# Optimization experiments

Hardware: AMD Instinct MI355X
Metric: run time of the kernel (lower is better)

Reference implementation:

```python
import jax, jax.numpy as jnp
import numpy as np
from jax import lax

B, E, D, N, R, K = 4, 768, 1536, 16, 48, 4
H, W = 16, 16
L = H * W
NDIR = 4


def _perms():
    idx = np.arange(L)
    idx_v = np.arange(L).reshape(H, W).T.reshape(-1)  # column-major (vertical) scan order
    perms = [idx, idx[::-1].copy(), idx_v, idx_v[::-1].copy()]
    invs = [np.argsort(p) for p in perms]
    return [jnp.asarray(p) for p in perms], [jnp.asarray(p) for p in invs]

PERMS, INVS = _perms()


def setup_inputs() -> dict:
    key = jax.random.key(0)
    ks = jax.random.split(key, 10)
    hidden_states = jax.random.normal(ks[0], (B, L, E), jnp.float32)
    in_proj_w = jax.random.normal(ks[1], (2 * D, E), jnp.float32) * 0.02
    out_proj_w = jax.random.normal(ks[2], (E, D), jnp.float32) * 0.02
    conv_w = jax.random.normal(ks[3], (NDIR, D, K), jnp.float32) * 0.1
    conv_b = jax.random.normal(ks[4], (NDIR, D), jnp.float32) * 0.1
    xproj_w = jax.random.normal(ks[5], (NDIR, R + 2 * N, D), jnp.float32) * 0.02
    dt_init_std = R ** -0.5
    dtproj_w = jax.random.uniform(ks[6], (NDIR, D, R), jnp.float32, -dt_init_std, dt_init_std)
    dt = jnp.exp(jax.random.uniform(ks[7], (NDIR, D), jnp.float32)
                 * (np.log(0.1) - np.log(0.001)) + np.log(0.001))
    dt = jnp.clip(dt, 1e-4, None)
    dtproj_b = dt + jnp.log(-jnp.expm1(-dt))  # inverse-softplus init as in the module
    A_log = jnp.broadcast_to(
        jnp.log(jnp.arange(1, N + 1, dtype=jnp.float32))[None, None, :], (NDIR, D, N)).copy()
    D_param = jnp.ones((NDIR, D), jnp.float32)
    return dict(hidden_states=hidden_states, in_proj_w=in_proj_w, out_proj_w=out_proj_w,
                conv_w=conv_w, conv_b=conv_b, xproj_w=xproj_w, dtproj_w=dtproj_w,
                dtproj_b=dtproj_b, A_log=A_log, D_param=D_param)


def _mamba_dir(xz, cw, cb, xw, dtw, dtb, a_log, dpar):
    # xz: (B, 2D, L) in this direction's scan order
    x, z = xz[:, :D], xz[:, D:]
    # causal depthwise conv1d + SiLU (mamba_inner_fn conv path)
    x = lax.conv_general_dilated(x, cw[:, None, :], (1,), [(K - 1, 0)],
                                 feature_group_count=D,
                                 dimension_numbers=('NCH', 'OIH', 'NCH'))
    x = jax.nn.silu(x + cb[None, :, None])
    # x_proj -> dt, B, C
    x_dbl = jnp.einsum('bdl,kd->bkl', x, xw)
    dt, Bm, Cm = x_dbl[:, :R], x_dbl[:, R:R + N], x_dbl[:, R + N:]
    delta = jax.nn.softplus(jnp.einsum('brl,dr->bdl', dt, dtw) + dtb[None, :, None])
    A = -jnp.exp(a_log)                                  # (D, N)
    dA = jnp.exp(jnp.einsum('bdl,dn->lbdn', delta, A))   # (L, B, D, N)
    dBu = jnp.einsum('bdl,bnl,bdl->lbdn', delta, Bm, x)  # delta * B * u

    def step(h, inp):
        da, dbu = inp
        h = da * h + dbu
        return h, h

    h0 = jnp.zeros((x.shape[0], D, N), x.dtype)
    _, hs = lax.scan(step, h0, (dA, dBu))                # (L, B, D, N)
    y = jnp.einsum('lbdn,bnl->bdl', hs, Cm) + dpar[None, :, None] * x
    return y * jax.nn.silu(z)                            # gate, (B, D, L)


def reference(hidden_states, in_proj_w, out_proj_w, conv_w, conv_b,
              xproj_w, dtproj_w, dtproj_b, A_log, D_param):
    xz = jnp.einsum('ble,fe->bfl', hidden_states, in_proj_w)  # (B, 2D, L)
    out = jnp.zeros((hidden_states.shape[0], D, L), hidden_states.dtype)
    for i in range(NDIR):  # fixed small set of structurally distinct scan directions
        xz_i = xz[:, :, PERMS[i]]
        y = _mamba_dir(xz_i, conv_w[i], conv_b[i], xproj_w[i], dtproj_w[i],
                       dtproj_b[i], A_log[i], D_param[i])
        out = out + y[:, :, INVS[i]]  # multi_reverse then sum-fusion
    return jnp.einsum('bdl,ed->ble', out, out_proj_w)
```

## Files before the change

### kernel.cpp

```cpp
#include <hip/hip_runtime.h>
#include <hip/hip_bf16.h>

#define BI   4
#define LI   256
#define EI   768
#define DI   1536
#define NI   16
#define RI   48
#define KI   4
#define NDIRS 4
#define F2D  3072
#define MROWS 1024
#define LOG2E 1.4426950408889634f

typedef float    floatx2 __attribute__((ext_vector_type(2)));
typedef float    floatx4 __attribute__((ext_vector_type(4)));
typedef _Float16 halfx2  __attribute__((ext_vector_type(2)));
typedef _Float16 halfx4  __attribute__((ext_vector_type(4)));
typedef _Float16 halfx8  __attribute__((ext_vector_type(8)));

typedef __attribute__((address_space(3))) unsigned lds_u32;
typedef __attribute__((address_space(1))) const unsigned glb_u32;

__device__ __forceinline__ void load16(const _Float16* g, _Float16* l) {
    __builtin_amdgcn_global_load_lds((glb_u32*)g, (lds_u32*)l, 16, 0, 0);
}

__device__ __forceinline__ int perm_idx(int dir, int j) {
    switch (dir) {
        case 0:  return j;
        case 1:  return 255 - j;
        case 2:  return ((j & 15) << 4) | (j >> 4);
        default: return 255 - (((j & 15) << 4) | (j >> 4));
    }
}

template<int CTRL>
__device__ __forceinline__ float dpp_add(float p) {
    int t = __builtin_amdgcn_update_dpp(0, __builtin_bit_cast(int, p),
                                        CTRL, 0xf, 0xf, true);
    return p + __builtin_bit_cast(float, t);
}
__device__ __forceinline__ float grp8_sum(float p) {
    p = dpp_add<0xB1>(p);
    p = dpp_add<0x4E>(p);
    p = dpp_add<0x141>(p);
    return p;
}

template<int BM, int BN, int WGN, int FM, int FN>
__device__ __forceinline__ void gemm_core(const _Float16* __restrict__ Ah,
                                          const _Float16* __restrict__ Al, int lda,
                                          const _Float16* __restrict__ Bh,
                                          const _Float16* __restrict__ Bl, int ldb,
                                          int nChunks, _Float16* smem,
                                          floatx4 (&acc)[FM][FN]) {
    const int tid = threadIdx.x, lane = tid & 63, wave = tid >> 6;
    const int wave_m = wave / WGN, wave_n = wave % WGN;
    _Float16* sAh = smem;
    _Float16* sAl = smem + BM * 32;
    _Float16* sBh = smem + BM * 64;
    _Float16* sBl = smem + BM * 64 + BN * 32;
    const int rr = lane & 15, koff = (lane >> 4) * 8;
    const int arow = wave_m * FM * 16, brow = wave_n * FN * 16;

    for (int c = 0; c < nChunks; ++c) {
        for (int idx = tid; idx < BM * 4; idx += 256) {
            int r = idx >> 2, s = (idx & 3) * 8;
            load16(Ah + (size_t)r * lda + c * 32 + s, sAh + idx * 8);
            load16(Al + (size_t)r * lda + c * 32 + s, sAl + idx * 8);
        }
        for (int idx = tid; idx < BN * 4; idx += 256) {
            int r = idx >> 2, s = (idx & 3) * 8;
            load16(Bh + (size_t)r * ldb + c * 32 + s, sBh + idx * 8);
            load16(Bl + (size_t)r * ldb + c * 32 + s, sBl + idx * 8);
        }
        asm volatile("s_waitcnt vmcnt(0)" ::: "memory");
        __syncthreads();

        halfx8 ahf[FM], alf[FM], bhf[FN], blf[FN];
        #pragma unroll
        for (int i = 0; i < FM; ++i) {
            ahf[i] = *(const halfx8*)(sAh + (arow + i * 16 + rr) * 32 + koff);
            alf[i] = *(const halfx8*)(sAl + (arow + i * 16 + rr) * 32 + koff);
        }
        #pragma unroll
        for (int j = 0; j < FN; ++j) {
            bhf[j] = *(const halfx8*)(sBh + (brow + j * 16 + rr) * 32 + koff);
            blf[j] = *(const halfx8*)(sBl + (brow + j * 16 + rr) * 32 + koff);
        }
        #pragma unroll
        for (int i = 0; i < FM; ++i)
            #pragma unroll
            for (int j = 0; j < FN; ++j) {
                acc[i][j] = __builtin_amdgcn_mfma_f32_16x16x32_f16(ahf[i], bhf[j], acc[i][j], 0, 0, 0);
                acc[i][j] = __builtin_amdgcn_mfma_f32_16x16x32_f16(ahf[i], blf[j], acc[i][j], 0, 0, 0);
                acc[i][j] = __builtin_amdgcn_mfma_f32_16x16x32_f16(alf[i], bhf[j], acc[i][j], 0, 0, 0);
            }
        __syncthreads();
    }
}

__global__ __launch_bounds__(256) void k_splitall(
        const float* __restrict__ hs,  const float* __restrict__ wip,
        const float* __restrict__ wop, const float* __restrict__ xw,
        const float* __restrict__ dtw,
        _Float16* __restrict__ hsh,  _Float16* __restrict__ hsl,
        _Float16* __restrict__ wiph, _Float16* __restrict__ wipl,
        _Float16* __restrict__ woph, _Float16* __restrict__ wopl,
        _Float16* __restrict__ xwh,  _Float16* __restrict__ xwl,
        _Float16* __restrict__ dtwh, _Float16* __restrict__ dtwl) {
    int i4 = (blockIdx.x * 256 + threadIdx.x) * 4;
    floatx4 v;
    _Float16 *dh, *dl; int off;
    if (i4 < 786432)        { off = i4;           v = *(const floatx4*)(hs + off);  dh = hsh;  dl = hsl;  }
    else if (i4 < 3145728)  { off = i4 - 786432;  v = *(const floatx4*)(wip + off); dh = wiph; dl = wipl; }
    else if (i4 < 4325376)  { off = i4 - 3145728; v = *(const floatx4*)(wop + off); dh = woph; dl = wopl; }
    else if (i4 < 4816896)  { off = i4 - 4325376; v = *(const floatx4*)(xw + off);  dh = xwh;  dl = xwl;  }
    else {
        int t0 = i4 - 4816896;
        int col = t0 & 63, dr = t0 >> 6;
        floatx4 z = {0.f, 0.f, 0.f, 0.f};
        v = (col < 48) ? *(const floatx4*)(dtw + (size_t)dr * 48 + col) : z;
        dh = dtwh; dl = dtwl; off = t0;
    }
    halfx4 hh, hl;
    #pragma unroll
    for (int e = 0; e < 4; ++e) {
        _Float16 h = (_Float16)v[e];
        hh[e] = h; hl[e] = (_Float16)(v[e] - (float)h);
    }
    *(halfx4*)(dh + off) = hh;
    *(halfx4*)(dl + off) = hl;
}

__global__ __launch_bounds__(256) void k_inproj_t(const _Float16* __restrict__ Ah,
                                                  const _Float16* __restrict__ Al,
                                                  const _Float16* __restrict__ Bh,
                                                  const _Float16* __restrict__ Bl,
                                                  float* __restrict__ C) {
    __shared__ _Float16 smem[128 * 64 + 128 * 64];
    int row0 = blockIdx.x * 128, col0 = blockIdx.y * 128, k0 = blockIdx.z * 384;
    float* Cp = C + (size_t)blockIdx.z * MROWS * F2D;
    floatx4 acc[4][4] = {};
    gemm_core<128, 128, 2, 4, 4>(Ah + (size_t)row0 * EI + k0, Al + (size_t)row0 * EI + k0, EI,
                                 Bh + (size_t)col0 * EI + k0, Bl + (size_t)col0 * EI + k0, EI,
                                 12, smem, acc);
    int lane = threadIdx.x & 63, wave = threadIdx.x >> 6;
    int cc = lane & 15, q = lane >> 4;
    int rbase = row0 + (wave >> 1) * 64, cbase = col0 + (wave & 1) * 64;
    #pragma unroll
    for (int i = 0; i < 4; ++i)
        #pragma unroll
        for (int j = 0; j < 4; ++j)
            #pragma unroll
            for (int r = 0; r < 4; ++r)
                Cp[(size_t)(rbase + i * 16 + q * 4 + r) * F2D + cbase + j * 16 + cc] = acc[i][j][r];
}

__global__ __launch_bounds__(256) void k_outproj_t(const _Float16* __restrict__ Ah,
                                                   const _Float16* __restrict__ Al,
                                                   const _Float16* __restrict__ Bh,
                                                   const _Float16* __restrict__ Bl,
                                                   float* __restrict__ C) {
    __shared__ _Float16 smem[192 * 64];
    int row0 = blockIdx.x * 64, col0 = blockIdx.y * 128, k0 = blockIdx.z * 384;
    float* Cp = C + (size_t)blockIdx.z * MROWS * EI;
    floatx4 acc[2][4] = {};
    gemm_core<64, 128, 2, 2, 4>(Ah + (size_t)row0 * DI + k0, Al + (size_t)row0 * DI + k0, DI,
                                Bh + (size_t)col0 * DI + k0, Bl + (size_t)col0 * DI + k0, DI,
                                12, smem, acc);
    int lane = threadIdx.x & 63, wave = threadIdx.x >> 6;
    int cc = lane & 15, q = lane >> 4;
    int rbase = row0 + (wave >> 1) * 32, cbase = col0 + (wave & 1) * 64;
    #pragma unroll
    for (int i = 0; i < 2; ++i)
        #pragma unroll
        for (int j = 0; j < 4; ++j)
            #pragma unroll
            for (int r = 0; r < 4; ++r)
                Cp[(size_t)(rbase + i * 16 + q * 4 + r) * EI + cbase + j * 16 + cc] = acc[i][j][r];
}

__global__ __launch_bounds__(256) void k_osum(const float* __restrict__ oacc,
                                              float* __restrict__ out) {
    int i4 = (blockIdx.x * 256 + threadIdx.x) * 4;
    const size_t S = (size_t)MROWS * EI;
    floatx4 s = *(const floatx4*)(oacc + i4) + *(const floatx4*)(oacc + S + i4) +
                *(const floatx4*)(oacc + 2 * S + i4) + *(const floatx4*)(oacc + 3 * S + i4);
    *(floatx4*)(out + i4) = s;
}

__global__ __launch_bounds__(256) void k_xdbl_t(const _Float16* __restrict__ xh,
                                                const _Float16* __restrict__ xl,
                                                const _Float16* __restrict__ xwh,
                                                const _Float16* __restrict__ xwl,
                                                float* __restrict__ C) {
    __shared__ _Float16 smem[208 * 64];
    int row0 = blockIdx.x * 128, dir = blockIdx.y, k0 = blockIdx.z * 192;
    float* Cp = C + (size_t)blockIdx.z * NDIRS * MROWS * 80;
    floatx4 acc[2][5] = {};
    const size_t abase = ((size_t)dir * MROWS + row0) * DI + k0;
    const size_t bbase = (size_t)dir * 80 * DI + k0;
    gemm_core<128, 80, 1, 2, 5>(xh + abase, xl + abase, DI,
                                xwh + bbase, xwl + bbase, DI, 6, smem, acc);
    int lane = threadIdx.x & 63, wave = threadIdx.x >> 6;
    int cc = lane & 15, q = lane >> 4;
    int rbase = row0 + wave * 32;
    #pragma unroll
    for (int i = 0; i < 2; ++i)
        #pragma unroll
        for (int j = 0; j < 5; ++j)
            #pragma unroll
            for (int r = 0; r < 4; ++r)
                Cp[((size_t)dir * MROWS + rbase + i * 16 + q * 4 + r) * 80 + j * 16 + cc] = acc[i][j][r];
}

__global__ __launch_bounds__(256) void k_xsplit(const float* __restrict__ acc,
                                                _Float16* __restrict__ dtqh,
                                                _Float16* __restrict__ dtql,
                                                float* __restrict__ BCm) {
    const size_t PS = (size_t)NDIRS * MROWS * 80;
    int idx = blockIdx.x * 256 + threadIdx.x;
    int dir = idx / (MROWS * 96);
    int rem = idx - dir * MROWS * 96;
    int row = rem / 96, col = rem - row * 96;
    size_t rbase = (size_t)dir * MROWS + row;
    auto sum8 = [&](int c) {
        size_t o = rbase * 80 + c;
        float s = 0.f;
        #pragma unroll
        for (int kp = 0; kp < 8; ++kp) s += acc[kp * PS + o];
        return s;
    };
    if (col < 64) {
        float v = (col < 48) ? sum8(col) : 0.f;
        _Float16 h = (_Float16)v;
        dtqh[rbase * 64 + col] = h;
        dtql[rbase * 64 + col] = (_Float16)(v - (float)h);
    } else if (col < 80) {
        int n = col - 64;
        BCm[rbase * 32 + n * 2] = sum8(48 + n);
    } else {
        int n = col - 80;
        BCm[rbase * 32 + n * 2 + 1] = sum8(64 + n);
    }
}

__global__ __launch_bounds__(256) void k_delta_t(const _Float16* __restrict__ dtqh,
                                                 const _Float16* __restrict__ dtql,
                                                 const _Float16* __restrict__ dtwh,
                                                 const _Float16* __restrict__ dtwl,
                                                 const float* __restrict__ dtb,
                                                 float* __restrict__ delta) {
    __shared__ _Float16 smem[192 * 64];
    int row0 = blockIdx.x * 64, col0 = blockIdx.y * 128, dir = blockIdx.z;
    floatx4 acc[2][4] = {};
    const size_t abase = ((size_t)dir * MROWS + row0) * 64;
    const size_t bbase = ((size_t)dir * DI + col0) * 64;
    gemm_core<64, 128, 2, 2, 4>(dtqh + abase, dtql + abase, 64,
                                dtwh + bbase, dtwl + bbase, 64, 2, smem, acc);
    int lane = threadIdx.x & 63, wave = threadIdx.x >> 6;
    int cc = lane & 15, q = lane >> 4;
    int rbase = row0 + (wave >> 1) * 32, cbase = col0 + (wave & 1) * 64;
    #pragma unroll
    for (int i = 0; i < 2; ++i)
        #pragma unroll
        for (int j = 0; j < 4; ++j) {
            int col = cbase + j * 16 + cc;
            float bias = dtb[(size_t)dir * DI + col];
            #pragma unroll
            for (int r = 0; r < 4; ++r) {
                float v = acc[i][j][r] + bias;
                float sp = (v > 20.f) ? v : log1pf(__expf(v));
                delta[((size_t)dir * MROWS + rbase + i * 16 + q * 4 + r) * DI + col] = sp;
            }
        }
}

__global__ __launch_bounds__(256) void k_conv(const float* __restrict__ xz,
                                              const float* __restrict__ cw,
                                              const float* __restrict__ cb,
                                              _Float16* __restrict__ xh,
                                              _Float16* __restrict__ xl) {
    const size_t S = (size_t)MROWS * F2D;
    int dir = blockIdx.z, b = blockIdx.y;
    int lchunk = blockIdx.x / 6, dsub = blockIdx.x % 6;
    int d = dsub * 256 + threadIdx.x;
    int base = lchunk * 16;

    const float* w = cw + ((size_t)dir * DI + d) * KI;
    float w0 = w[0], w1 = w[1], w2 = w[2], w3 = w[3];
    float bias = cb[(size_t)dir * DI + d];

    auto ld = [&](int m) -> float {
        if (m < 0) return 0.f;
        int src = perm_idx(dir, m);
        size_t o = ((size_t)b * 256 + src) * F2D + d;
        return xz[o] + xz[S + o];
    };
    float xm3 = ld(base - 3), xm2 = ld(base - 2), xm1 = ld(base - 1);

    #pragma unroll
    for (int j = 0; j < 16; ++j) {
        float cur = ld(base + j);
        float s = bias + w0 * xm3 + w1 * xm2 + w2 * xm1 + w3 * cur;
        xm3 = xm2; xm2 = xm1; xm1 = cur;
        float x = s / (1.f + __expf(-s));
        _Float16 h = (_Float16)x;
        size_t o = ((size_t)dir * MROWS + b * 256 + base + j) * DI + d;
        xh[o] = h;
        xl[o] = (_Float16)(x - (float)h);
    }
}

__global__ __launch_bounds__(256) void k_scan(const float* __restrict__ delta,
                                              const _Float16* __restrict__ xhg,
                                              const _Float16* __restrict__ xlg,
                                              const float* __restrict__ BCm,
                                              const float* __restrict__ A_log,
                                              const float* __restrict__ Dp,
                                              float* __restrict__ ydir) {
    const int dchunk = blockIdx.x, b = blockIdx.y, dir = blockIdx.z;
    const int tid = threadIdx.x;
    const int dslot = tid >> 3;
    const int np = tid & 7;
    const int d0 = dchunk * 32, d = d0 + dslot;

    __shared__ float sdx[2][32][64];
    __shared__ float sbc[2][32][32];

    const float Av0 = -__expf(A_log[((size_t)dir * DI + d) * NI + 2 * np]) * LOG2E;
    const float Av1 = -__expf(A_log[((size_t)dir * DI + d) * NI + 2 * np + 1]) * LOG2E;
    const float Dpar = Dp[(size_t)dir * DI + d];
    float h0 = 0.f, h1 = 0.f;

    const size_t dirrow = (size_t)dir * MROWS;
    const int srow = tid >> 3, sc4 = (tid & 7) * 4;

    floatx4 rdel, rbc;
    halfx4 rxh, rxl;
    auto load_chunk = [&](int j0) {
        int row = b * 256 + j0 + srow;
        size_t o = (dirrow + row) * DI + d0 + sc4;
        rdel = *(const floatx4*)(delta + o);
        rxh  = *(const halfx4*)(xhg + o);
        rxl  = *(const halfx4*)(xlg + o);
        rbc  = *(const floatx4*)(BCm + (dirrow + row) * 32 + sc4);
    };

    load_chunk(0);

    for (int c = 0; c < 8; ++c) {
        const int buf = c & 1;
        #pragma unroll
        for (int e = 0; e < 4; ++e) {
            sdx[buf][srow][(sc4 + e) * 2]     = rdel[e];
            sdx[buf][srow][(sc4 + e) * 2 + 1] = (float)rxh[e] + (float)rxl[e];
        }
        *(floatx4*)&sbc[buf][srow][sc4] = rbc;
        __syncthreads();
        if (c < 7) load_chunk((c + 1) * 32);

        #pragma unroll
        for (int jj = 0; jj < 32; ++jj) {
            floatx2 dx = *(const floatx2*)&sdx[buf][jj][dslot * 2];
            floatx4 bc = *(const floatx4*)&sbc[buf][jj][np * 4];
            float dv = dx[0], xv = dx[1];
            float a0 = __builtin_amdgcn_exp2f(dv * Av0);
            float a1 = __builtin_amdgcn_exp2f(dv * Av1);
            float du = dv * xv;
            h0 = fmaf(a0, h0, du * bc[0]);
            h1 = fmaf(a1, h1, du * bc[2]);
            float p = fmaf(h1, bc[3], h0 * bc[1]);
            p = grp8_sum(p);
            if (np == 0) {
                int lout = perm_idx(dir, c * 32 + jj);
                ydir[(dirrow + (size_t)b * 256 + lout) * DI + d] = fmaf(Dpar, xv, p);
            }
        }
    }
}

__global__ __launch_bounds__(256) void k_sum(const float* __restrict__ ydir,
                                             const float* __restrict__ xz,
                                             _Float16* __restrict__ yh,
                                             _Float16* __restrict__ yl) {
    int i4 = (blockIdx.x * 256 + threadIdx.x) * 4;
    const size_t S = (size_t)MROWS * DI;
    const size_t SZ = (size_t)MROWS * F2D;
    int row = i4 / DI, dcol = i4 - row * DI;
    size_t zo = (size_t)row * F2D + DI + dcol;
    floatx4 zv = *(const floatx4*)(xz + zo) + *(const floatx4*)(xz + SZ + zo);
    floatx4 s = *(const floatx4*)(ydir + i4) + *(const floatx4*)(ydir + S + i4) +
                *(const floatx4*)(ydir + 2 * S + i4) + *(const floatx4*)(ydir + 3 * S + i4);
    halfx4 hh, hl;
    #pragma unroll
    for (int e = 0; e < 4; ++e) {
        float g = zv[e] / (1.f + __expf(-zv[e]));
        float v = s[e] * g;
        _Float16 h = (_Float16)v;
        hh[e] = h; hl[e] = (_Float16)(v - (float)h);
    }
    *(halfx4*)(yh + i4) = hh;
    *(halfx4*)(yl + i4) = hl;
}

extern "C" void kernel_launch(void* const* d_in, const int* in_sizes, int n_in,
                              void* d_out, int out_size, void* d_ws, size_t ws_size,
                              hipStream_t stream) {
    const float* hs   = (const float*)d_in[0];
    const float* wip  = (const float*)d_in[1];
    const float* wop  = (const float*)d_in[2];
    const float* cw   = (const float*)d_in[3];
    const float* cb   = (const float*)d_in[4];
    const float* xw   = (const float*)d_in[5];
    const float* dtw  = (const float*)d_in[6];
    const float* dtb  = (const float*)d_in[7];
    const float* alog = (const float*)d_in[8];
    const float* dpar = (const float*)d_in[9];
    float* out = (float*)d_out;

    char* p = (char*)d_ws;
    auto alloc_f32 = [&](size_t n) { float* r = (float*)p; p += n * 4; return r; };
    auto alloc_f16 = [&](size_t n) { _Float16* r = (_Float16*)p; p += n * 2; return r; };

    _Float16* hsh  = alloc_f16(786432);
    _Float16* hsl  = alloc_f16(786432);
    _Float16* wiph = alloc_f16(2359296);
    _Float16* wipl = alloc_f16(2359296);
    _Float16* woph = alloc_f16(1179648);
    _Float16* wopl = alloc_f16(1179648);
    _Float16* xwh  = alloc_f16(491520);
    _Float16* xwl  = alloc_f16(491520);
    _Float16* dtwh = alloc_f16((size_t)NDIRS * DI * 64);
    _Float16* dtwl = alloc_f16((size_t)NDIRS * DI * 64);
    float*    xz   = alloc_f32((size_t)2 * MROWS * F2D);
    _Float16* xh   = alloc_f16((size_t)NDIRS * MROWS * DI);
    _Float16* xl   = alloc_f16((size_t)NDIRS * MROWS * DI);
    _Float16* dtqh = alloc_f16((size_t)NDIRS * MROWS * 64);
    _Float16* dtql = alloc_f16((size_t)NDIRS * MROWS * 64);
    float*    BCm  = alloc_f32((size_t)NDIRS * MROWS * 32);
    float*    delta= alloc_f32((size_t)NDIRS * MROWS * DI);
    float*    ydir = alloc_f32((size_t)NDIRS * MROWS * DI);
    _Float16* yh   = alloc_f16((size_t)MROWS * DI);
    _Float16* yl   = alloc_f16((size_t)MROWS * DI);

    float* xdba = ydir;
    float* oacc = delta;

    k_splitall<<<dim3(5088), 256, 0, stream>>>(hs, wip, wop, xw, dtw,
                                               hsh, hsl, wiph, wipl, woph, wopl,
                                               xwh, xwl, dtwh, dtwl);
    k_inproj_t<<<dim3(8, 24, 2), 256, 0, stream>>>(hsh, hsl, wiph, wipl, xz);
    k_conv    <<<dim3(96, BI, NDIRS), 256, 0, stream>>>(xz, cw, cb, xh, xl);
    k_xdbl_t  <<<dim3(8, NDIRS, 8), 256, 0, stream>>>(xh, xl, xwh, xwl, xdba);
    k_xsplit  <<<dim3(1536), 256, 0, stream>>>(xdba, dtqh, dtql, BCm);
    k_delta_t <<<dim3(16, 12, NDIRS), 256, 0, stream>>>(dtqh, dtql, dtwh, dtwl, dtb, delta);
    k_scan    <<<dim3(DI / 32, BI, NDIRS), 256, 0, stream>>>(delta, xh, xl, BCm,
                                                             alog, dpar, ydir);
    k_sum     <<<dim3(1536), 256, 0, stream>>>(ydir, xz, yh, yl);
    k_outproj_t<<<dim3(16, 6, 4), 256, 0, stream>>>(yh, yl, woph, wopl, oacc);
    k_osum    <<<dim3(768), 256, 0, stream>>>(oacc, out);
}
```

Baseline: 245.0 us.

## Drop split-K in in-proj GEMM and stage scan outputs for coalesced stores

The input-projection GEMM no longer splits K into two partial buffers. It uses 64x128 tiles over the full K, which doubles the grid in M and removes the partial-sum reads in the conv and gating kernels. The scan kernel now collects each 32-step chunk of outputs in shared memory and writes them as row-wise vector stores, replacing scattered single-float stores. The cost is an extra barrier per chunk and a longer K loop per GEMM block.

```diff
diff --git a/kernel.cpp b/kernel.cpp
--- a/kernel.cpp
+++ b/kernel.cpp
@@ -139,23 +139,22 @@
                                                   const _Float16* __restrict__ Bh,
                                                   const _Float16* __restrict__ Bl,
                                                   float* __restrict__ C) {
-    __shared__ _Float16 smem[128 * 64 + 128 * 64];
-    int row0 = blockIdx.x * 128, col0 = blockIdx.y * 128, k0 = blockIdx.z * 384;
-    float* Cp = C + (size_t)blockIdx.z * MROWS * F2D;
-    floatx4 acc[4][4] = {};
-    gemm_core<128, 128, 2, 4, 4>(Ah + (size_t)row0 * EI + k0, Al + (size_t)row0 * EI + k0, EI,
-                                 Bh + (size_t)col0 * EI + k0, Bl + (size_t)col0 * EI + k0, EI,
-                                 12, smem, acc);
+    __shared__ _Float16 smem[192 * 64];
+    int row0 = blockIdx.x * 64, col0 = blockIdx.y * 128;
+    floatx4 acc[2][4] = {};
+    gemm_core<64, 128, 2, 2, 4>(Ah + (size_t)row0 * EI, Al + (size_t)row0 * EI, EI,
+                                Bh + (size_t)col0 * EI, Bl + (size_t)col0 * EI, EI,
+                                EI / 32, smem, acc);
     int lane = threadIdx.x & 63, wave = threadIdx.x >> 6;
     int cc = lane & 15, q = lane >> 4;
-    int rbase = row0 + (wave >> 1) * 64, cbase = col0 + (wave & 1) * 64;
-    #pragma unroll
-    for (int i = 0; i < 4; ++i)
+    int rbase = row0 + (wave >> 1) * 32, cbase = col0 + (wave & 1) * 64;
+    #pragma unroll
+    for (int i = 0; i < 2; ++i)
         #pragma unroll
         for (int j = 0; j < 4; ++j)
             #pragma unroll
             for (int r = 0; r < 4; ++r)
-                Cp[(size_t)(rbase + i * 16 + q * 4 + r) * F2D + cbase + j * 16 + cc] = acc[i][j][r];
+                C[(size_t)(rbase + i * 16 + q * 4 + r) * F2D + cbase + j * 16 + cc] = acc[i][j][r];
 }
 
 __global__ __launch_bounds__(256) void k_outproj_t(const _Float16* __restrict__ Ah,
@@ -283,7 +282,6 @@
                                               const float* __restrict__ cb,
                                               _Float16* __restrict__ xh,
                                               _Float16* __restrict__ xl) {
-    const size_t S = (size_t)MROWS * F2D;
     int dir = blockIdx.z, b = blockIdx.y;
     int lchunk = blockIdx.x / 6, dsub = blockIdx.x % 6;
     int d = dsub * 256 + threadIdx.x;
@@ -296,8 +294,7 @@
     auto ld = [&](int m) -> float {
         if (m < 0) return 0.f;
         int src = perm_idx(dir, m);
-        size_t o = ((size_t)b * 256 + src) * F2D + d;
-        return xz[o] + xz[S + o];
+        return xz[((size_t)b * 256 + src) * F2D + d];
     };
     float xm3 = ld(base - 3), xm2 = ld(base - 2), xm1 = ld(base - 1);
 
@@ -329,6 +326,7 @@
 
     __shared__ float sdx[2][32][64];
     __shared__ float sbc[2][32][32];
+    __shared__ float sY[32][32];
 
     const float Av0 = -__expf(A_log[((size_t)dir * DI + d) * NI + 2 * np]) * LOG2E;
     const float Av1 = -__expf(A_log[((size_t)dir * DI + d) * NI + 2 * np + 1]) * LOG2E;
@@ -374,10 +372,14 @@
             h1 = fmaf(a1, h1, du * bc[2]);
             float p = fmaf(h1, bc[3], h0 * bc[1]);
             p = grp8_sum(p);
-            if (np == 0) {
-                int lout = perm_idx(dir, c * 32 + jj);
-                ydir[(dirrow + (size_t)b * 256 + lout) * DI + d] = fmaf(Dpar, xv, p);
-            }
+            if (np == 0) sY[jj][dslot] = fmaf(Dpar, xv, p);
+        }
+        __syncthreads();
+
+        {
+            int lout = perm_idx(dir, c * 32 + srow);
+            floatx4 o = *(const floatx4*)&sY[srow][sc4];
+            *(floatx4*)&ydir[(dirrow + (size_t)b * 256 + lout) * DI + d0 + sc4] = o;
         }
     }
 }
@@ -388,10 +390,8 @@
                                              _Float16* __restrict__ yl) {
     int i4 = (blockIdx.x * 256 + threadIdx.x) * 4;
     const size_t S = (size_t)MROWS * DI;
-    const size_t SZ = (size_t)MROWS * F2D;
     int row = i4 / DI, dcol = i4 - row * DI;
-    size_t zo = (size_t)row * F2D + DI + dcol;
-    floatx4 zv = *(const floatx4*)(xz + zo) + *(const floatx4*)(xz + SZ + zo);
+    floatx4 zv = *(const floatx4*)(xz + (size_t)row * F2D + DI + dcol);
     floatx4 s = *(const floatx4*)(ydir + i4) + *(const floatx4*)(ydir + S + i4) +
                 *(const floatx4*)(ydir + 2 * S + i4) + *(const floatx4*)(ydir + 3 * S + i4);
     halfx4 hh, hl;
@@ -435,7 +435,7 @@
     _Float16* xwl  = alloc_f16(491520);
     _Float16* dtwh = alloc_f16((size_t)NDIRS * DI * 64);
     _Float16* dtwl = alloc_f16((size_t)NDIRS * DI * 64);
-    float*    xz   = alloc_f32((size_t)2 * MROWS * F2D);
+    float*    xz   = alloc_f32((size_t)MROWS * F2D);
     _Float16* xh   = alloc_f16((size_t)NDIRS * MROWS * DI);
     _Float16* xl   = alloc_f16((size_t)NDIRS * MROWS * DI);
     _Float16* dtqh = alloc_f16((size_t)NDIRS * MROWS * 64);
@@ -452,7 +452,7 @@
     k_splitall<<<dim3(5088), 256, 0, stream>>>(hs, wip, wop, xw, dtw,
                                                hsh, hsl, wiph, wipl, woph, wopl,
                                                xwh, xwl, dtwh, dtwl);
-    k_inproj_t<<<dim3(8, 24, 2), 256, 0, stream>>>(hsh, hsl, wiph, wipl, xz);
+    k_inproj_t<<<dim3(16, 24), 256, 0, stream>>>(hsh, hsl, wiph, wipl, xz);
     k_conv    <<<dim3(96, BI, NDIRS), 256, 0, stream>>>(xz, cw, cb, xh, xl);
     k_xdbl_t  <<<dim3(8, NDIRS, 8), 256, 0, stream>>>(xh, xl, xwh, xwl, xdba);
     k_xsplit  <<<dim3(1536), 256, 0, stream>>>(xdba, dtqh, dtql, BCm);
```

New measurement: 230.0 us. 1.07x faster.
